# Performance work log

Hardware: AMD Instinct MI355X
Metric: run time of the kernel (lower is better)

## Reference

```python
import jax, jax.numpy as jnp
import numpy as np

B, T, N, F = 32, 36, 10000, 3
HORIZON = 10
NUM_REGIONS = 20
NAN_RATE = 0.05


def setup_inputs() -> dict:
    key = jax.random.key(0)
    k1, k2, k3 = jax.random.split(key, 3)
    seq = jax.random.normal(k1, (B, T, N, F), dtype=jnp.float32)
    nan_mask = jax.random.uniform(k2, (B, T, N, F)) < NAN_RATE
    seq = jnp.where(nan_mask, jnp.nan, seq)
    cluster_id = jax.random.randint(k3, (N,), 0, NUM_REGIONS, dtype=jnp.int64)
    return {"seq": seq, "cluster_id": cluster_id}


def _nanmean_all(x):
    valid = ~jnp.isnan(x)
    s = jnp.where(valid, x, 0.0).sum()
    c = valid.sum().astype(x.dtype)
    return s / c


def reference(seq, cluster_id):
    x = seq[..., 0]                               # [B, T, N] speed channel
    valid = ~jnp.isnan(x)
    xz = jnp.where(valid, x, 0.0)
    cnt = valid.sum(axis=1).astype(x.dtype)       # [B, N]
    time_mean = xz.sum(axis=1) / cnt              # [B, N]; NaN if a node is all-NaN
    pred_speed = jnp.tile(time_mean[:, None, :], (1, HORIZON, 1))  # [B, 10, N]

    # per-region nanmean over nodes: segment-mean via one-hot contraction
    onehot = (cluster_id[:, None] == jnp.arange(NUM_REGIONS)).astype(x.dtype)  # [N, R]
    pvalid = ~jnp.isnan(pred_speed)
    pz = jnp.where(pvalid, pred_speed, 0.0)
    rsum = jnp.einsum('bhn,nr->bhr', pz, onehot)                     # [B, 10, R]
    rcnt = jnp.einsum('bhn,nr->bhr', pvalid.astype(x.dtype), onehot)  # [B, 10, R]
    regional = rsum / rcnt                                            # NaN if region all-NaN

    # nan_to_global_avg: replace remaining NaNs with global nanmean of each tensor
    g1 = _nanmean_all(pred_speed)
    g2 = _nanmean_all(regional)
    out_pred = jnp.where(jnp.isnan(pred_speed), g1, pred_speed)
    out_regional = jnp.where(jnp.isnan(regional), g2, regional)
    return out_pred, out_regional
```

## Files before the change

kernel.cpp:

```cpp
#include <hip/hip_runtime.h>

#define BB 32
#define TT 36
#define NN 10000
#define FF 3
#define HH 10
#define RR 20
#define NQ (NN / 4)


__global__ __launch_bounds__(256) void k_time_mean(
        const float* __restrict__ seq,
        const int* __restrict__ cid,
        float* __restrict__ tm,
        float* __restrict__ rsum,
        float* __restrict__ rcnt,
        float* __restrict__ gsum,
        float* __restrict__ gcnt) {
    __shared__ float ls[RR];
    __shared__ float lc[RR];
    const int b = blockIdx.y;
    const int q = blockIdx.x * blockDim.x + threadIdx.x;
    if (threadIdx.x < RR) { ls[threadIdx.x] = 0.f; lc[threadIdx.x] = 0.f; }
    __syncthreads();

    float lsum = 0.f, lcnt = 0.f;

    if (q < NQ) {
        const float4* p = (const float4*)seq + (size_t)b * TT * NN * FF / 4 + 3 * q;
        const size_t tstride = (size_t)NN * FF / 4;
        float s0 = 0.f, s1 = 0.f, s2 = 0.f, s3 = 0.f;
        int c0 = 0, c1 = 0, c2 = 0, c3 = 0;
        #pragma unroll
        for (int t = 0; t < TT; ++t) {
            float4 q0 = p[0];
            float4 q1 = p[1];
            float4 q2 = p[2];
            p += tstride;
            float v0 = q0.x, v1 = q0.w, v2 = q1.z, v3 = q2.y;
            if (v0 == v0) { s0 += v0; c0++; }
            if (v1 == v1) { s1 += v1; c1++; }
            if (v2 == v2) { s2 += v2; c2++; }
            if (v3 == v3) { s3 += v3; c3++; }
        }
        const float nanf_ = __int_as_float(0x7fc00000);
        float m0 = c0 ? s0 / (float)c0 : nanf_;
        float m1 = c1 ? s1 / (float)c1 : nanf_;
        float m2 = c2 ? s2 / (float)c2 : nanf_;
        float m3 = c3 ? s3 / (float)c3 : nanf_;
        ((float4*)tm)[(size_t)b * NQ + q] = make_float4(m0, m1, m2, m3);

        const int4 r4 = ((const int4*)cid)[q];
        if (c0) { atomicAdd(&ls[r4.x], m0); atomicAdd(&lc[r4.x], 1.f); lsum += m0; lcnt += 1.f; }
        if (c1) { atomicAdd(&ls[r4.y], m1); atomicAdd(&lc[r4.y], 1.f); lsum += m1; lcnt += 1.f; }
        if (c2) { atomicAdd(&ls[r4.z], m2); atomicAdd(&lc[r4.z], 1.f); lsum += m2; lcnt += 1.f; }
        if (c3) { atomicAdd(&ls[r4.w], m3); atomicAdd(&lc[r4.w], 1.f); lsum += m3; lcnt += 1.f; }
    }

    for (int off = 32; off > 0; off >>= 1) {
        lsum += __shfl_down(lsum, off, 64);
        lcnt += __shfl_down(lcnt, off, 64);
    }
    if ((threadIdx.x & 63) == 0) {
        atomicAdd(gsum, lsum);
        atomicAdd(gcnt, lcnt);
    }

    __syncthreads();
    if (threadIdx.x < RR) {
        atomicAdd(&rsum[b * RR + threadIdx.x], ls[threadIdx.x]);
        atomicAdd(&rcnt[b * RR + threadIdx.x], lc[threadIdx.x]);
    }
}

__global__ void k_regional(const float* __restrict__ rsum,
                           const float* __restrict__ rcnt,
                           const float* __restrict__ gsum,
                           const float* __restrict__ gcnt,
                           float* __restrict__ g1out,
                           float* __restrict__ out_reg) {
    const int tid = threadIdx.x;
    __shared__ float ssum[10];
    __shared__ float scnt[10];
    __shared__ float g2s;

    float val = 0.f;
    int valid = 0;
    if (tid < BB * RR) {
        float c = rcnt[tid];
        if (c > 0.f) { val = rsum[tid] / c; valid = 1; }
    }

    float wsv = valid ? val : 0.f;
    float wcv = (float)valid;
    for (int off = 32; off > 0; off >>= 1) {
        wsv += __shfl_down(wsv, off, 64);
        wcv += __shfl_down(wcv, off, 64);
    }
    const int wave = tid >> 6;
    if ((tid & 63) == 0) { ssum[wave] = wsv; scnt[wave] = wcv; }
    __syncthreads();

    if (tid == 0) {
        float s = 0.f, c = 0.f;
        #pragma unroll
        for (int i = 0; i < 10; ++i) { s += ssum[i]; c += scnt[i]; }
        g2s = s / c;
        g1out[0] = gsum[0] / gcnt[0];
    }
    __syncthreads();

    if (tid < BB * RR) {
        const int b = tid / RR, r = tid % RR;
        const float o = valid ? val : g2s;
        #pragma unroll
        for (int h = 0; h < HH; ++h)
            out_reg[(size_t)(b * HH + h) * RR + r] = o;
    }
}

__global__ __launch_bounds__(256) void k_pred(
        const float* __restrict__ tm,
        const float* __restrict__ g1p,
        float* __restrict__ out) {
    const int b = blockIdx.y;
    const int q = blockIdx.x * blockDim.x + threadIdx.x;
    if (q >= NQ) return;
    const float g1 = g1p[0];
    float4 v = ((const float4*)tm)[(size_t)b * NQ + q];
    if (!(v.x == v.x)) v.x = g1;
    if (!(v.y == v.y)) v.y = g1;
    if (!(v.z == v.z)) v.z = g1;
    if (!(v.w == v.w)) v.w = g1;
    float4* o = (float4*)out + (size_t)b * HH * NQ + q;
    #pragma unroll
    for (int h = 0; h < HH; ++h)
        o[(size_t)h * NQ] = v;
}

extern "C" void kernel_launch(void* const* d_in, const int* in_sizes, int n_in,
                              void* d_out, int out_size, void* d_ws, size_t ws_size,
                              hipStream_t stream) {
    const float* seq = (const float*)d_in[0];
    const int*   cid = (const int*)d_in[1];
    float* out = (float*)d_out;

    float* ws   = (float*)d_ws;
    float* tm   = ws;
    float* rsum = tm + BB * NN;
    float* rcnt = rsum + BB * RR;
    float* gsum = rcnt + BB * RR;
    float* gcnt = gsum + 1;
    float* g1   = gcnt + 1;

    hipMemsetAsync(rsum, 0, (size_t)(2 * BB * RR + 2) * sizeof(float), stream);

    dim3 blk(256);
    dim3 grd((NQ + 255) / 256, BB);
    k_time_mean<<<grd, blk, 0, stream>>>(seq, cid, tm, rsum, rcnt, gsum, gcnt);
    k_regional<<<1, 640, 0, stream>>>(rsum, rcnt, gsum, gcnt, g1,
                                      out + (size_t)BB * HH * NN);
    k_pred<<<grd, blk, 0, stream>>>(tm, g1, out);
}
```

Baseline: 232.6 us.

## Split time reduction into chunked partial-sum kernel plus finishing kernel

The time-mean reduction is split across 6 time chunks in a new kernel, so the grid is six times larger and more loads are in flight on the memory system. Per-chunk partial sums and counts go to workspace, and a second kernel combines them, computes the means and performs the regional and global atomics. This exposes more parallelism for the bandwidth-bound read of seq. The cost is an extra kernel launch and roughly 15 MB of extra workspace traffic for the partials.

```diff
diff --git a/kernel.cpp b/kernel.cpp
--- a/kernel.cpp
+++ b/kernel.cpp
@@ -7,10 +7,42 @@
 #define HH 10
 #define RR 20
 #define NQ (NN / 4)
+#define TCH 6
+#define TSTEPS 6
 
 
-__global__ __launch_bounds__(256) void k_time_mean(
+__global__ __launch_bounds__(256) void k_partial(
         const float* __restrict__ seq,
+        float4* __restrict__ psum,
+        float4* __restrict__ pcnt) {
+    const int b = blockIdx.y, tch = blockIdx.z;
+    const int q = blockIdx.x * blockDim.x + threadIdx.x;
+    if (q >= NQ) return;
+    const float4* p = (const float4*)seq
+        + (size_t)(b * TT + tch * TSTEPS) * (NN * FF / 4) + 3 * q;
+    const size_t tstride = NN * FF / 4;
+    float s0 = 0.f, s1 = 0.f, s2 = 0.f, s3 = 0.f;
+    float c0 = 0.f, c1 = 0.f, c2 = 0.f, c3 = 0.f;
+    #pragma unroll
+    for (int t = 0; t < TSTEPS; ++t) {
+        float4 a0 = p[0];
+        float4 a1 = p[1];
+        float4 a2 = p[2];
+        p += tstride;
+        float v0 = a0.x, v1 = a0.w, v2 = a1.z, v3 = a2.y;
+        if (v0 == v0) { s0 += v0; c0 += 1.f; }
+        if (v1 == v1) { s1 += v1; c1 += 1.f; }
+        if (v2 == v2) { s2 += v2; c2 += 1.f; }
+        if (v3 == v3) { s3 += v3; c3 += 1.f; }
+    }
+    const size_t o = (size_t)(tch * BB + b) * NQ + q;
+    psum[o] = make_float4(s0, s1, s2, s3);
+    pcnt[o] = make_float4(c0, c1, c2, c3);
+}
+
+__global__ __launch_bounds__(256) void k_finish(
+        const float4* __restrict__ psum,
+        const float4* __restrict__ pcnt,
         const int* __restrict__ cid,
         float* __restrict__ tm,
         float* __restrict__ rsum,
@@ -25,36 +57,29 @@
     __syncthreads();
 
     float lsum = 0.f, lcnt = 0.f;
-
     if (q < NQ) {
-        const float4* p = (const float4*)seq + (size_t)b * TT * NN * FF / 4 + 3 * q;
-        const size_t tstride = (size_t)NN * FF / 4;
         float s0 = 0.f, s1 = 0.f, s2 = 0.f, s3 = 0.f;
-        int c0 = 0, c1 = 0, c2 = 0, c3 = 0;
+        float c0 = 0.f, c1 = 0.f, c2 = 0.f, c3 = 0.f;
         #pragma unroll
-        for (int t = 0; t < TT; ++t) {
-            float4 q0 = p[0];
-            float4 q1 = p[1];
-            float4 q2 = p[2];
-            p += tstride;
-            float v0 = q0.x, v1 = q0.w, v2 = q1.z, v3 = q2.y;
-            if (v0 == v0) { s0 += v0; c0++; }
-            if (v1 == v1) { s1 += v1; c1++; }
-            if (v2 == v2) { s2 += v2; c2++; }
-            if (v3 == v3) { s3 += v3; c3++; }
+        for (int tch = 0; tch < TCH; ++tch) {
+            const size_t o = (size_t)(tch * BB + b) * NQ + q;
+            float4 ps = psum[o];
+            float4 pc = pcnt[o];
+            s0 += ps.x; s1 += ps.y; s2 += ps.z; s3 += ps.w;
+            c0 += pc.x; c1 += pc.y; c2 += pc.z; c3 += pc.w;
         }
         const float nanf_ = __int_as_float(0x7fc00000);
-        float m0 = c0 ? s0 / (float)c0 : nanf_;
-        float m1 = c1 ? s1 / (float)c1 : nanf_;
-        float m2 = c2 ? s2 / (float)c2 : nanf_;
-        float m3 = c3 ? s3 / (float)c3 : nanf_;
+        float m0 = (c0 > 0.f) ? s0 / c0 : nanf_;
+        float m1 = (c1 > 0.f) ? s1 / c1 : nanf_;
+        float m2 = (c2 > 0.f) ? s2 / c2 : nanf_;
+        float m3 = (c3 > 0.f) ? s3 / c3 : nanf_;
         ((float4*)tm)[(size_t)b * NQ + q] = make_float4(m0, m1, m2, m3);
 
         const int4 r4 = ((const int4*)cid)[q];
-        if (c0) { atomicAdd(&ls[r4.x], m0); atomicAdd(&lc[r4.x], 1.f); lsum += m0; lcnt += 1.f; }
-        if (c1) { atomicAdd(&ls[r4.y], m1); atomicAdd(&lc[r4.y], 1.f); lsum += m1; lcnt += 1.f; }
-        if (c2) { atomicAdd(&ls[r4.z], m2); atomicAdd(&lc[r4.z], 1.f); lsum += m2; lcnt += 1.f; }
-        if (c3) { atomicAdd(&ls[r4.w], m3); atomicAdd(&lc[r4.w], 1.f); lsum += m3; lcnt += 1.f; }
+        if (c0 > 0.f) { atomicAdd(&ls[r4.x], m0); atomicAdd(&lc[r4.x], 1.f); lsum += m0; lcnt += 1.f; }
+        if (c1 > 0.f) { atomicAdd(&ls[r4.y], m1); atomicAdd(&lc[r4.y], 1.f); lsum += m1; lcnt += 1.f; }
+        if (c2 > 0.f) { atomicAdd(&ls[r4.z], m2); atomicAdd(&lc[r4.z], 1.f); lsum += m2; lcnt += 1.f; }
+        if (c3 > 0.f) { atomicAdd(&ls[r4.w], m3); atomicAdd(&lc[r4.w], 1.f); lsum += m3; lcnt += 1.f; }
     }
 
     for (int off = 32; off > 0; off >>= 1) {
@@ -145,20 +170,24 @@
     const int*   cid = (const int*)d_in[1];
     float* out = (float*)d_out;
 
-    float* ws   = (float*)d_ws;
-    float* tm   = ws;
-    float* rsum = tm + BB * NN;
-    float* rcnt = rsum + BB * RR;
-    float* gsum = rcnt + BB * RR;
-    float* gcnt = gsum + 1;
-    float* g1   = gcnt + 1;
+    float*  ws   = (float*)d_ws;
+    float4* psum = (float4*)ws;
+    float4* pcnt = psum + (size_t)TCH * BB * NQ;
+    float*  tm   = (float*)(pcnt + (size_t)TCH * BB * NQ);
+    float*  rsum = tm + (size_t)BB * NN;
+    float*  rcnt = rsum + BB * RR;
+    float*  gsum = rcnt + BB * RR;
+    float*  gcnt = gsum + 1;
+    float*  g1   = gcnt + 1;
 
     hipMemsetAsync(rsum, 0, (size_t)(2 * BB * RR + 2) * sizeof(float), stream);
 
     dim3 blk(256);
-    dim3 grd((NQ + 255) / 256, BB);
-    k_time_mean<<<grd, blk, 0, stream>>>(seq, cid, tm, rsum, rcnt, gsum, gcnt);
+    dim3 grdA((NQ + 255) / 256, BB, TCH);
+    dim3 grdB((NQ + 255) / 256, BB);
+    k_partial<<<grdA, blk, 0, stream>>>(seq, psum, pcnt);
+    k_finish<<<grdB, blk, 0, stream>>>(psum, pcnt, cid, tm, rsum, rcnt, gsum, gcnt);
     k_regional<<<1, 640, 0, stream>>>(rsum, rcnt, gsum, gcnt, g1,
                                       out + (size_t)BB * HH * NN);
-    k_pred<<<grd, blk, 0, stream>>>(tm, g1, out);
+    k_pred<<<grdB, blk, 0, stream>>>(tm, g1, out);
 }
```

Measured after the change: 249.0 us. 7.0% more time.
